# Kernel optimization log

Hardware: AMD Instinct MI355X
Metric: run time of the kernel (lower is better)

## Reference

```python
import jax, jax.numpy as jnp
import numpy as np

B, S, F = 32, 4096, 256
G, N = 2, 128           # num_groups, num_entries_per_group
D = F // G              # group_dim = 128
E = 256                 # embed_dim


def setup_inputs() -> dict:
    key = jax.random.key(0)
    ks = jax.random.split(key, 6)
    return {
        "features": jax.random.normal(ks[0], (B, S, F), jnp.float32),
        "gumbel": jax.random.gumbel(ks[1], (B, S, G, N), jnp.float32),
        "W_logits": jax.random.normal(ks[2], (G, D, N), jnp.float32) * (1.0 / np.sqrt(D)),
        "b_logits": jnp.zeros((G, N), jnp.float32),
        "codebooks": jax.random.normal(ks[3], (G, N, D), jnp.float32) * 0.02,
        "W_out": jax.random.normal(ks[4], (F, E), jnp.float32) * (1.0 / np.sqrt(F)),
        "b_out": jnp.zeros((E,), jnp.float32),
    }


def reference(features, gumbel, W_logits, b_logits, codebooks, W_out, b_out):
    b, s, f = features.shape
    grouped = features.reshape(b, s, G, D)                       # [B,S,G,D]
    logits = jnp.einsum("bsgd,gdn->bsgn", grouped, W_logits) + b_logits
    noisy = logits + gumbel                                      # training=True
    soft = jax.nn.softmax(noisy, axis=-1)                        # [B,S,G,N]
    hard_idx = jnp.argmax(noisy, axis=-1)                        # [B,S,G] int
    hard = jax.nn.one_hot(hard_idx, N, dtype=soft.dtype)
    st = jax.lax.stop_gradient(hard - soft) + soft               # straight-through
    quantized = jnp.einsum("bsgn,gnd->bsgd", st, codebooks)      # [B,S,G,D]
    quantized = quantized.reshape(b, s, G * D)                   # [B,S,F]
    out = quantized @ W_out + b_out                              # [B,S,E]
    indices = hard_idx.astype(jnp.int32)                         # [B,S,G]
    return out, indices
```

## Files before the change

kernel.cpp:

```cpp
#include <hip/hip_runtime.h>

#define T_TOTAL (32 * 4096)
#define FDIM 256
#define NG 2
#define NN 128
#define DDIM 128
#define EDIM 256

#define TAU 0.004f
#define CAP 16384

typedef __attribute__((ext_vector_type(4))) float f32x4;
typedef __attribute__((ext_vector_type(8))) short short8;

__global__ __launch_bounds__(256) void prep_kernel(
    const float* __restrict__ codebooks,
    const float* __restrict__ W_out,
    const float* __restrict__ Wl,
    float* __restrict__ CO,
    short* __restrict__ BT,
    int* __restrict__ flag_count)
{
    const int gn  = blockIdx.x;
    const int g   = gn >> 7;
    const int tid = threadIdx.x;
    __shared__ float cb[DDIM];
    if (tid < DDIM) cb[tid] = codebooks[gn * DDIM + tid];
    if (tid >= 128) {
        const int k = tid - 128;
        const int n = gn & 127;
        const float x = Wl[((size_t)g * DDIM + k) * NN + n];
        const unsigned u = __float_as_uint(x);
        const float hi = __uint_as_float(u & 0xffff0000u);
        const unsigned u2 = __float_as_uint(x - hi);
        BT[(size_t)g * 16384 + n * 128 + k] = (short)(u >> 16);
        BT[32768 + (size_t)g * 16384 + n * 128 + k] = (short)(u2 >> 16);
    }
    if (gn == 0 && tid == 0) *flag_count = 0;
    __syncthreads();
    float acc = 0.f;
    const float* wcol = W_out + (g * DDIM) * EDIM + tid;
#pragma unroll 4
    for (int d = 0; d < DDIM; ++d) acc += cb[d] * wcol[d * EDIM];
    CO[gn * EDIM + tid] = acc;
}

__global__ __launch_bounds__(512) void pq_v11_kernel(
    const float* __restrict__ features,
    const float* __restrict__ gumbel,
    const short* __restrict__ BT,
    const float* __restrict__ bl,
    float* __restrict__ idx_f,
    int* __restrict__ flag_count,
    int* __restrict__ flag_list)
{
    __shared__ short8 Flds[2048];
    __shared__ float pm1s[8][64];
    __shared__ float pm2s[8][64];
    __shared__ int   pi1s[8][64];

    const int tid  = threadIdx.x;
    const int g    = blockIdx.x & 1;
    const int span = blockIdx.x >> 1;
    const int w    = tid >> 6;
    const int l    = tid & 63;
    const int q    = l & 15;
    const int h    = l >> 4;
    const int n0   = w * 16;
    const int tb0  = span * 256;

    const short* bt1 = BT + (size_t)g * 16384 + (n0 + q) * 128 + h * 8;
    short8 A1[4], A2[4];
#pragma unroll
    for (int ks = 0; ks < 4; ++ks) {
        A1[ks] = *reinterpret_cast<const short8*>(bt1 + ks * 32);
        A2[ks] = *reinterpret_cast<const short8*>(bt1 + 32768 + ks * 32);
    }
    const f32x4 bv = *reinterpret_cast<const f32x4*>(bl + g * NN + n0 + h * 4);

    const int stok = tid >> 3;
    const int skc  = tid & 7;
    const int swz  = stok & 7;

    for (int st = 0; st < 4; ++st) {
        const int t64 = tb0 + st * 64;

        const float* fp = features + (size_t)(t64 + stok) * FDIM + g * DDIM + skc * 16;
        const f32x4 F0 = *reinterpret_cast<const f32x4*>(fp);
        const f32x4 F1 = *reinterpret_cast<const f32x4*>(fp + 4);
        const f32x4 F2 = *reinterpret_cast<const f32x4*>(fp + 8);
        const f32x4 F3 = *reinterpret_cast<const f32x4*>(fp + 12);

        short8 SH0, SH1, SL0, SL1;
#pragma unroll
        for (int e = 0; e < 4; ++e) {
            unsigned u; float hi;
            u = __float_as_uint(F0[e]); hi = __uint_as_float(u & 0xffff0000u);
            SH0[e]     = (short)(u >> 16); SL0[e]     = (short)(__float_as_uint(F0[e] - hi) >> 16);
            u = __float_as_uint(F1[e]); hi = __uint_as_float(u & 0xffff0000u);
            SH0[4 + e] = (short)(u >> 16); SL0[4 + e] = (short)(__float_as_uint(F1[e] - hi) >> 16);
            u = __float_as_uint(F2[e]); hi = __uint_as_float(u & 0xffff0000u);
            SH1[e]     = (short)(u >> 16); SL1[e]     = (short)(__float_as_uint(F2[e] - hi) >> 16);
            u = __float_as_uint(F3[e]); hi = __uint_as_float(u & 0xffff0000u);
            SH1[4 + e] = (short)(u >> 16); SL1[4 + e] = (short)(__float_as_uint(F3[e] - hi) >> 16);
        }

        __syncthreads();

        if (st > 0 && tid < 64) {
            float c1 = pm1s[0][tid], c2 = pm2s[0][tid];
            int   ci = pi1s[0][tid];
#pragma unroll
            for (int p = 1; p < 8; ++p) {
                const float a1 = pm1s[p][tid];
                const float a2 = pm2s[p][tid];
                const int   ai = pi1s[p][tid];
                if (a1 > c1)      { c2 = fmaxf(c1, a2); c1 = a1; ci = ai; }
                else if (a1 < c1) { c2 = fmaxf(c2, a1); }
                else              { c2 = c1; ci = min(ci, ai); }
            }
            const int t = tb0 + (st - 1) * 64 + tid;
            idx_f[(size_t)t * NG + g] = (float)ci;
            if (c1 - c2 < TAU) {
                const int p = atomicAdd(flag_count, 1);
                if (p < CAP) flag_list[p] = t * NG + g;
            }
        }

        {
            short8* rowHi = Flds + stok * 16;
            short8* rowLo = Flds + 1024 + stok * 16;
            rowHi[(2 * skc)     ^ swz] = SH0;
            rowHi[(2 * skc + 1) ^ swz] = SH1;
            rowLo[(2 * skc)     ^ swz] = SL0;
            rowLo[(2 * skc + 1) ^ swz] = SL1;
        }
        __syncthreads();

        for (int s = 0; s < 4; ++s) {
            const int t = t64 + s * 16 + q;
            const f32x4 G = *reinterpret_cast<const f32x4*>(
                gumbel + ((size_t)t * NG + g) * NN + n0 + h * 4);

            const int rbase = (s * 16 + q) * 16;
            f32x4 acc = (f32x4){0.f, 0.f, 0.f, 0.f};
#pragma unroll
            for (int ks = 0; ks < 4; ++ks) {
                const int ci0 = (ks * 4 + h) ^ (q & 7);
                const short8 B1 = Flds[rbase + ci0];
                const short8 B2 = Flds[1024 + rbase + ci0];
                acc = __builtin_amdgcn_mfma_f32_16x16x32_bf16(A1[ks], B1, acc, 0, 0, 0);
                acc = __builtin_amdgcn_mfma_f32_16x16x32_bf16(A2[ks], B1, acc, 0, 0, 0);
                acc = __builtin_amdgcn_mfma_f32_16x16x32_bf16(A1[ks], B2, acc, 0, 0, 0);
            }

            float m1 = -3.4e38f, m2 = -3.4e38f;
            int   i1 = 0;
#pragma unroll
            for (int r = 0; r < 4; ++r) {
                const float vv = acc[r] + bv[r] + G[r];
                const int   n  = n0 + h * 4 + r;
                if (vv > m1) { m2 = m1; m1 = vv; i1 = n; }
                else         { m2 = fmaxf(m2, vv); }
            }
#pragma unroll
            for (int off = 16; off < 64; off <<= 1) {
                const float om1 = __shfl_xor(m1, off);
                const int   oi1 = __shfl_xor(i1, off);
                const float om2 = __shfl_xor(m2, off);
                if (om1 > m1)      { m2 = fmaxf(m1, om2); m1 = om1; i1 = oi1; }
                else if (om1 < m1) { m2 = fmaxf(m2, om1); }
                else               { m2 = m1; i1 = min(i1, oi1); }
            }
            if (h == 0) {
                pm1s[w][s * 16 + q] = m1;
                pm2s[w][s * 16 + q] = m2;
                pi1s[w][s * 16 + q] = i1;
            }
        }
    }

    __syncthreads();
    if (tid < 64) {
        float c1 = pm1s[0][tid], c2 = pm2s[0][tid];
        int   ci = pi1s[0][tid];
#pragma unroll
        for (int p = 1; p < 8; ++p) {
            const float a1 = pm1s[p][tid];
            const float a2 = pm2s[p][tid];
            const int   ai = pi1s[p][tid];
            if (a1 > c1)      { c2 = fmaxf(c1, a2); c1 = a1; ci = ai; }
            else if (a1 < c1) { c2 = fmaxf(c2, a1); }
            else              { c2 = c1; ci = min(ci, ai); }
        }
        const int t = tb0 + 3 * 64 + tid;
        idx_f[(size_t)t * NG + g] = (float)ci;
        if (c1 - c2 < TAU) {
            const int p = atomicAdd(flag_count, 1);
            if (p < CAP) flag_list[p] = t * NG + g;
        }
    }
}

__global__ __launch_bounds__(128) void fixup_kernel(
    const float* __restrict__ features,
    const float* __restrict__ gumbel,
    const float* __restrict__ Wl,
    const float* __restrict__ bl,
    float* __restrict__ idx_f,
    const int* __restrict__ flag_count,
    const int* __restrict__ flag_list)
{
    __shared__ float sm[2];
    __shared__ int   si[2];
    int total = *flag_count;
    if (total > CAP) total = CAP;
    const int n = threadIdx.x;

    for (int e = blockIdx.x; e < total; e += gridDim.x) {
        const int code = flag_list[e];
        const int t = code >> 1, g = code & 1;
        const float* fpr = features + (size_t)t * FDIM + g * DDIM;
        const float* wp  = Wl + (size_t)g * DDIM * NN + n;
        float dot = 0.f;
#pragma unroll 8
        for (int k = 0; k < DDIM; ++k) dot = fmaf(fpr[k], wp[(size_t)k * NN], dot);
        const float v = (dot + bl[g * NN + n]) + gumbel[((size_t)t * NG + g) * NN + n];

        float m = v; int bi = n;
#pragma unroll
        for (int off = 1; off < 64; off <<= 1) {
            const float om = __shfl_xor(m, off);
            const int   ob = __shfl_xor(bi, off);
            if (om > m || (om == m && ob < bi)) { m = om; bi = ob; }
        }
        if ((n & 63) == 0) { sm[n >> 6] = m; si[n >> 6] = bi; }
        __syncthreads();
        if (n == 0) {
            const float mA = sm[0], mB = sm[1];
            const int bA = si[0], bB = si[1];
            const int best = (mB > mA || (mB == mA && bB < bA)) ? bB : bA;
            idx_f[code] = (float)best;
        }
        __syncthreads();
    }
}

__global__ __launch_bounds__(256) void out_kernel(
    const float* __restrict__ CO,
    const float* __restrict__ b_out,
    const float* __restrict__ idx_f,
    float* __restrict__ out)
{
    const int tid = threadIdx.x;
    const int e4  = tid & 63;
    const int ts  = tid >> 6;
    const int tbase = blockIdx.x * 16;
    const float4 b = *reinterpret_cast<const float4*>(b_out + e4 * 4);

#pragma unroll
    for (int it = 0; it < 4; ++it) {
        const int t  = tbase + it * 4 + ts;
        const int i0 = (int)idx_f[t * NG + 0];
        const int i1 = (int)idx_f[t * NG + 1];
        const float4 c0 = *reinterpret_cast<const float4*>(CO + (size_t)i0 * EDIM + e4 * 4);
        const float4 c1 = *reinterpret_cast<const float4*>(CO + (size_t)(NN + i1) * EDIM + e4 * 4);
        float4 o;
        o.x = c0.x + c1.x + b.x;
        o.y = c0.y + c1.y + b.y;
        o.z = c0.z + c1.z + b.z;
        o.w = c0.w + c1.w + b.w;
        *reinterpret_cast<float4*>(out + (size_t)t * EDIM + e4 * 4) = o;
    }
}

extern "C" void kernel_launch(void* const* d_in, const int* in_sizes, int n_in,
                              void* d_out, int out_size, void* d_ws, size_t ws_size,
                              hipStream_t stream) {
    const float* features  = (const float*)d_in[0];
    const float* gumbel    = (const float*)d_in[1];
    const float* Wl        = (const float*)d_in[2];
    const float* bl        = (const float*)d_in[3];
    const float* codebooks = (const float*)d_in[4];
    const float* W_out     = (const float*)d_in[5];
    const float* b_out     = (const float*)d_in[6];

    float* out   = (float*)d_out;
    float* idx_f = out + (size_t)T_TOTAL * EDIM;

    char* ws = (char*)d_ws;
    float* CO         = (float*)ws;
    short* BT         = (short*)(ws + 262144);
    int*   flag_count = (int*)(ws + 262144 + 131072);
    int*   flag_list  = (int*)(ws + 393216 + 256);

    prep_kernel<<<NG * NN, 256, 0, stream>>>(codebooks, W_out, Wl, CO, BT, flag_count);
    pq_v11_kernel<<<1024, 512, 0, stream>>>(
        features, gumbel, BT, bl, idx_f, flag_count, flag_list);
    fixup_kernel<<<1024, 128, 0, stream>>>(
        features, gumbel, Wl, bl, idx_f, flag_count, flag_list);
    out_kernel<<<T_TOTAL / 16, 256, 0, stream>>>(CO, b_out, idx_f, out);
}
```

Before: 132.3 us.

## Double-buffer features and gumbel into LDS via async global_load_lds

```diff
diff --git a/kernel.cpp b/kernel.cpp
--- a/kernel.cpp
+++ b/kernel.cpp
@@ -12,6 +12,13 @@
 
 typedef __attribute__((ext_vector_type(4))) float f32x4;
 typedef __attribute__((ext_vector_type(8))) short short8;
+
+__device__ __forceinline__ void gl2lds(const float* gsrc, float* ldst) {
+    __builtin_amdgcn_global_load_lds(
+        (const __attribute__((address_space(1))) unsigned int*)gsrc,
+        (__attribute__((address_space(3))) unsigned int*)ldst,
+        16, 0, 0);
+}
 
 __global__ __launch_bounds__(256) void prep_kernel(
     const float* __restrict__ codebooks,
@@ -45,7 +52,7 @@
     CO[gn * EDIM + tid] = acc;
 }
 
-__global__ __launch_bounds__(512) void pq_v11_kernel(
+__global__ __launch_bounds__(512) void pq_v20_kernel(
     const float* __restrict__ features,
     const float* __restrict__ gumbel,
     const short* __restrict__ BT,
@@ -54,20 +61,21 @@
     int* __restrict__ flag_count,
     int* __restrict__ flag_list)
 {
-    __shared__ short8 Flds[2048];
-    __shared__ float pm1s[8][64];
-    __shared__ float pm2s[8][64];
-    __shared__ int   pi1s[8][64];
-
-    const int tid  = threadIdx.x;
-    const int g    = blockIdx.x & 1;
-    const int span = blockIdx.x >> 1;
-    const int w    = tid >> 6;
-    const int l    = tid & 63;
-    const int q    = l & 15;
-    const int h    = l >> 4;
-    const int n0   = w * 16;
-    const int tb0  = span * 256;
+    __shared__ __align__(16) float Fb[2][32 * 128];
+    __shared__ __align__(16) float Gb[2][32 * 128];
+    __shared__ float pm1[2][8][32];
+    __shared__ float pm2[2][8][32];
+    __shared__ int   pi1[2][8][32];
+
+    const int tid = threadIdx.x;
+    const int g   = blockIdx.x & 1;
+    const int gb  = blockIdx.x >> 1;
+    const int w   = tid >> 6;
+    const int l   = tid & 63;
+    const int q   = l & 15;
+    const int h   = l >> 4;
+    const int n0  = w * 16;
+    const int tb0 = gb * 256;
 
     const short* bt1 = BT + (size_t)g * 16384 + (n0 + q) * 128 + h * 8;
     short8 A1[4], A2[4];
@@ -78,48 +86,45 @@
     }
     const f32x4 bv = *reinterpret_cast<const f32x4*>(bl + g * NN + n0 + h * 4);
 
-    const int stok = tid >> 3;
-    const int skc  = tid & 7;
-    const int swz  = stok & 7;
-
-    for (int st = 0; st < 4; ++st) {
-        const int t64 = tb0 + st * 64;
-
-        const float* fp = features + (size_t)(t64 + stok) * FDIM + g * DDIM + skc * 16;
-        const f32x4 F0 = *reinterpret_cast<const f32x4*>(fp);
-        const f32x4 F1 = *reinterpret_cast<const f32x4*>(fp + 4);
-        const f32x4 F2 = *reinterpret_cast<const f32x4*>(fp + 8);
-        const f32x4 F3 = *reinterpret_cast<const f32x4*>(fp + 12);
-
-        short8 SH0, SH1, SL0, SL1;
-#pragma unroll
-        for (int e = 0; e < 4; ++e) {
-            unsigned u; float hi;
-            u = __float_as_uint(F0[e]); hi = __uint_as_float(u & 0xffff0000u);
-            SH0[e]     = (short)(u >> 16); SL0[e]     = (short)(__float_as_uint(F0[e] - hi) >> 16);
-            u = __float_as_uint(F1[e]); hi = __uint_as_float(u & 0xffff0000u);
-            SH0[4 + e] = (short)(u >> 16); SL0[4 + e] = (short)(__float_as_uint(F1[e] - hi) >> 16);
-            u = __float_as_uint(F2[e]); hi = __uint_as_float(u & 0xffff0000u);
-            SH1[e]     = (short)(u >> 16); SL1[e]     = (short)(__float_as_uint(F2[e] - hi) >> 16);
-            u = __float_as_uint(F3[e]); hi = __uint_as_float(u & 0xffff0000u);
-            SH1[4 + e] = (short)(u >> 16); SL1[4 + e] = (short)(__float_as_uint(F3[e] - hi) >> 16);
-        }
-
+    const int r0 = 4 * w + (l >> 5);
+    const int r1 = r0 + 2;
+    const int cc = l & 31;
+    const float* fsrc0 = features + (size_t)(tb0 + r0) * FDIM + g * DDIM + ((cc ^ (r0 & 7)) << 2);
+    const float* fsrc1 = features + (size_t)(tb0 + r1) * FDIM + g * DDIM + ((cc ^ (r1 & 7)) << 2);
+    const float* gsrc0 = gumbel + ((size_t)(tb0 + r0) * NG + g) * NN + ((cc ^ (r0 & 7)) << 2);
+    const float* gsrc1 = gumbel + ((size_t)(tb0 + r1) * NG + g) * NN + ((cc ^ (r1 & 7)) << 2);
+
+#define STAGE(BUF, ST) do {                                                 \
+        const size_t fo = (size_t)(ST) * 32 * FDIM;                         \
+        const size_t go = (size_t)(ST) * 32 * (NG * NN);                    \
+        gl2lds(fsrc0 + fo, &Fb[BUF][(w * 2) * 256]);                        \
+        gl2lds(fsrc1 + fo, &Fb[BUF][(w * 2 + 1) * 256]);                    \
+        gl2lds(gsrc0 + go, &Gb[BUF][(w * 2) * 256]);                        \
+        gl2lds(gsrc1 + go, &Gb[BUF][(w * 2 + 1) * 256]);                    \
+    } while (0)
+
+    STAGE(0, 0);
+
+    for (int st = 0; st < 8; ++st) {
         __syncthreads();
 
-        if (st > 0 && tid < 64) {
-            float c1 = pm1s[0][tid], c2 = pm2s[0][tid];
-            int   ci = pi1s[0][tid];
+        const int cur = st & 1;
+        if (st < 7) STAGE(cur ^ 1, st + 1);
+
+        if (st > 0 && tid < 32) {
+            const int bufp = (st - 1) & 1;
+            float c1 = pm1[bufp][0][tid], c2 = pm2[bufp][0][tid];
+            int   ci = pi1[bufp][0][tid];
 #pragma unroll
             for (int p = 1; p < 8; ++p) {
-                const float a1 = pm1s[p][tid];
-                const float a2 = pm2s[p][tid];
-                const int   ai = pi1s[p][tid];
+                const float a1 = pm1[bufp][p][tid];
+                const float a2 = pm2[bufp][p][tid];
+                const int   ai = pi1[bufp][p][tid];
                 if (a1 > c1)      { c2 = fmaxf(c1, a2); c1 = a1; ci = ai; }
                 else if (a1 < c1) { c2 = fmaxf(c2, a1); }
                 else              { c2 = c1; ci = min(ci, ai); }
             }
-            const int t = tb0 + (st - 1) * 64 + tid;
+            const int t = tb0 + (st - 1) * 32 + tid;
             idx_f[(size_t)t * NG + g] = (float)ci;
             if (c1 - c2 < TAU) {
                 const int p = atomicAdd(flag_count, 1);
@@ -127,38 +132,42 @@
             }
         }
 
-        {
-            short8* rowHi = Flds + stok * 16;
-            short8* rowLo = Flds + 1024 + stok * 16;
-            rowHi[(2 * skc)     ^ swz] = SH0;
-            rowHi[(2 * skc + 1) ^ swz] = SH1;
-            rowLo[(2 * skc)     ^ swz] = SL0;
-            rowLo[(2 * skc + 1) ^ swz] = SL1;
-        }
-        __syncthreads();
-
-        for (int s = 0; s < 4; ++s) {
-            const int t = t64 + s * 16 + q;
-            const f32x4 G = *reinterpret_cast<const f32x4*>(
-                gumbel + ((size_t)t * NG + g) * NN + n0 + h * 4);
-
-            const int rbase = (s * 16 + q) * 16;
+#pragma unroll
+        for (int s = 0; s < 2; ++s) {
+            const int tl = s * 16 + q;
+            const int sw = tl & 7;
             f32x4 acc = (f32x4){0.f, 0.f, 0.f, 0.f};
 #pragma unroll
             for (int ks = 0; ks < 4; ++ks) {
-                const int ci0 = (ks * 4 + h) ^ (q & 7);
-                const short8 B1 = Flds[rbase + ci0];
-                const short8 B2 = Flds[1024 + rbase + ci0];
+                const f32x4 fa = *reinterpret_cast<const f32x4*>(
+                    &Fb[cur][tl * 128 + (((ks * 8 + h * 2)     ^ sw) << 2)]);
+                const f32x4 fb = *reinterpret_cast<const f32x4*>(
+                    &Fb[cur][tl * 128 + (((ks * 8 + h * 2 + 1) ^ sw) << 2)]);
+                short8 B1, B2;
+#pragma unroll
+                for (int e = 0; e < 4; ++e) {
+                    unsigned u = __float_as_uint(fa[e]);
+                    float hi = __uint_as_float(u & 0xffff0000u);
+                    B1[e] = (short)(u >> 16);
+                    B2[e] = (short)(__float_as_uint(fa[e] - hi) >> 16);
+                    u = __float_as_uint(fb[e]);
+                    hi = __uint_as_float(u & 0xffff0000u);
+                    B1[4 + e] = (short)(u >> 16);
+                    B2[4 + e] = (short)(__float_as_uint(fb[e] - hi) >> 16);
+                }
                 acc = __builtin_amdgcn_mfma_f32_16x16x32_bf16(A1[ks], B1, acc, 0, 0, 0);
                 acc = __builtin_amdgcn_mfma_f32_16x16x32_bf16(A2[ks], B1, acc, 0, 0, 0);
                 acc = __builtin_amdgcn_mfma_f32_16x16x32_bf16(A1[ks], B2, acc, 0, 0, 0);
             }
 
+            const f32x4 gvv = *reinterpret_cast<const f32x4*>(
+                &Gb[cur][tl * 128 + (((w * 4 + h) ^ sw) << 2)]);
+
             float m1 = -3.4e38f, m2 = -3.4e38f;
             int   i1 = 0;
 #pragma unroll
             for (int r = 0; r < 4; ++r) {
-                const float vv = acc[r] + bv[r] + G[r];
+                const float vv = acc[r] + bv[r] + gvv[r];
                 const int   n  = n0 + h * 4 + r;
                 if (vv > m1) { m2 = m1; m1 = vv; i1 = n; }
                 else         { m2 = fmaxf(m2, vv); }
@@ -173,27 +182,28 @@
                 else               { m2 = m1; i1 = min(i1, oi1); }
             }
             if (h == 0) {
-                pm1s[w][s * 16 + q] = m1;
-                pm2s[w][s * 16 + q] = m2;
-                pi1s[w][s * 16 + q] = i1;
-            }
-        }
-    }
+                pm1[cur][w][tl] = m1;
+                pm2[cur][w][tl] = m2;
+                pi1[cur][w][tl] = i1;
+            }
+        }
+    }
+#undef STAGE
 
     __syncthreads();
-    if (tid < 64) {
-        float c1 = pm1s[0][tid], c2 = pm2s[0][tid];
-        int   ci = pi1s[0][tid];
+    if (tid < 32) {
+        float c1 = pm1[1][0][tid], c2 = pm2[1][0][tid];
+        int   ci = pi1[1][0][tid];
 #pragma unroll
         for (int p = 1; p < 8; ++p) {
-            const float a1 = pm1s[p][tid];
-            const float a2 = pm2s[p][tid];
-            const int   ai = pi1s[p][tid];
+            const float a1 = pm1[1][p][tid];
+            const float a2 = pm2[1][p][tid];
+            const int   ai = pi1[1][p][tid];
             if (a1 > c1)      { c2 = fmaxf(c1, a2); c1 = a1; ci = ai; }
             else if (a1 < c1) { c2 = fmaxf(c2, a1); }
             else              { c2 = c1; ci = min(ci, ai); }
         }
-        const int t = tb0 + 3 * 64 + tid;
+        const int t = tb0 + 7 * 32 + tid;
         idx_f[(size_t)t * NG + g] = (float)ci;
         if (c1 - c2 < TAU) {
             const int p = atomicAdd(flag_count, 1);
@@ -219,6 +229,7 @@
 
     for (int e = blockIdx.x; e < total; e += gridDim.x) {
         const int code = flag_list[e];
+        if ((unsigned)code >= (unsigned)(T_TOTAL * NG)) continue;
         const int t = code >> 1, g = code & 1;
         const float* fpr = features + (size_t)t * FDIM + g * DDIM;
         const float* wp  = Wl + (size_t)g * DDIM * NN + n;
@@ -261,8 +272,8 @@
 #pragma unroll
     for (int it = 0; it < 4; ++it) {
         const int t  = tbase + it * 4 + ts;
-        const int i0 = (int)idx_f[t * NG + 0];
-        const int i1 = (int)idx_f[t * NG + 1];
+        const int i0 = ((int)idx_f[t * NG + 0]) & 127;
+        const int i1 = ((int)idx_f[t * NG + 1]) & 127;
         const float4 c0 = *reinterpret_cast<const float4*>(CO + (size_t)i0 * EDIM + e4 * 4);
         const float4 c1 = *reinterpret_cast<const float4*>(CO + (size_t)(NN + i1) * EDIM + e4 * 4);
         float4 o;
@@ -295,7 +306,7 @@
     int*   flag_list  = (int*)(ws + 393216 + 256);
 
     prep_kernel<<<NG * NN, 256, 0, stream>>>(codebooks, W_out, Wl, CO, BT, flag_count);
-    pq_v11_kernel<<<1024, 512, 0, stream>>>(
+    pq_v20_kernel<<<1024, 512, 0, stream>>>(
         features, gumbel, BT, bl, idx_f, flag_count, flag_list);
     fixup_kernel<<<1024, 128, 0, stream>>>(
         features, gumbel, Wl, bl, idx_f, flag_count, flag_list);
```

Result: slower. 136.7 us (+3.4%).
